# Optimization experiments

Measured on AMD Instinct MI355X. Metric: run time of the kernel, lower is better.

## Reference

```python
import jax, jax.numpy as jnp
import numpy as np

EMBED_DIM = 1024
NUM_HEADS = 16
BLOCK_SIZE = 128
GLOBAL_EVERY = 24


def make_block_sparse_mask(seq_len):
    # 0 where allowed, -inf where disallowed. Allowed iff same block, or
    # either position lies in a 'global' block (block index % global_every == 0).
    bi = jnp.arange(seq_len) // BLOCK_SIZE
    is_global = (bi % GLOBAL_EVERY) == 0
    allowed = (bi[:, None] == bi[None, :]) | is_global[:, None] | is_global[None, :]
    return jnp.where(allowed, 0.0, -jnp.inf).astype(jnp.float32)


def setup_inputs() -> dict:
    key = jax.random.key(0)
    k_x, k_w, k_wo = jax.random.split(key, 3)
    B, L, D = 1, 4096, EMBED_DIM
    x = jax.random.normal(k_x, (B, L, D), dtype=jnp.float32)
    # nn.MultiheadAttention params: packed in_proj [3D, D] + bias [3D], out_proj [D, D] + bias [D]
    w_qkv = jax.random.normal(k_w, (3 * D, D), dtype=jnp.float32) * 0.02
    b_qkv = jnp.zeros((3 * D,), dtype=jnp.float32)
    w_out = jax.random.normal(k_wo, (D, D), dtype=jnp.float32) * 0.02
    b_out = jnp.zeros((D,), dtype=jnp.float32)
    return {"x": x, "w_qkv": w_qkv, "b_qkv": b_qkv, "w_out": w_out, "b_out": b_out}


def reference(x, w_qkv, b_qkv, w_out, b_out):
    B, L, D = x.shape
    H = NUM_HEADS
    hd = D // H
    mask = make_block_sparse_mask(L)  # [L, L] additive
    qkv = x @ w_qkv.T + b_qkv  # [B, L, 3D]
    q, k, v = jnp.split(qkv, 3, axis=-1)
    # [B, H, L, hd]
    q = q.reshape(B, L, H, hd).transpose(0, 2, 1, 3)
    k = k.reshape(B, L, H, hd).transpose(0, 2, 1, 3)
    v = v.reshape(B, L, H, hd).transpose(0, 2, 1, 3)
    scale = 1.0 / jnp.sqrt(jnp.asarray(hd, dtype=x.dtype))
    scores = jnp.einsum('bhqd,bhkd->bhqk', q * scale, k) + mask  # [B, H, L, L]
    attn = jax.nn.softmax(scores, axis=-1)
    out = jnp.einsum('bhqk,bhkd->bhqd', attn, v)  # [B, H, L, hd]
    out = out.transpose(0, 2, 1, 3).reshape(B, L, D)
    return out @ w_out.T + b_out
```

## Files before the change

### kernel.cpp

```cpp
#include <hip/hip_runtime.h>
#include <hip/hip_bf16.h>
#include <math.h>


#define SEQ 4096
#define DIM 1024
#define NHEADS 16
#define HDIM 64
#define BS 128
#define ESTRIDE 136

using short8 = __attribute__((ext_vector_type(8))) short;
using floatx4 = __attribute__((ext_vector_type(4))) float;

__device__ __forceinline__ float bf2f(short s) {
  unsigned u = ((unsigned)(unsigned short)s) << 16;
  return __uint_as_float(u);
}

__device__ __forceinline__ unsigned pack_bf16(float a, float b) {
  __hip_bfloat16 ba = __float2bfloat16(a);
  __hip_bfloat16 bb = __float2bfloat16(b);
  return ((unsigned)*(unsigned short*)&bb << 16) | (unsigned)*(unsigned short*)&ba;
}

__device__ __forceinline__ void gld_lds16(const __hip_bfloat16* g, __hip_bfloat16* l) {
  __builtin_amdgcn_global_load_lds(
      (const __attribute__((address_space(1))) unsigned int*)g,
      (__attribute__((address_space(3))) unsigned int*)l, 16, 0, 0);
}

__global__ __launch_bounds__(256) void downcast3(
    const float* __restrict__ x, const float* __restrict__ wq,
    const float* __restrict__ wo, __hip_bfloat16* __restrict__ xd,
    __hip_bfloat16* __restrict__ wqd, __hip_bfloat16* __restrict__ wod) {
  int id = blockIdx.x;
  const float* src;
  __hip_bfloat16* dst;
  int base;
  if (id < 4096) { src = x; dst = xd; base = id; }
  else if (id < 7168) { src = wq; dst = wqd; base = id - 4096; }
  else { src = wo; dst = wod; base = id - 7168; }
  int i = (base * 256 + threadIdx.x) * 4;
  float4 v = *(const float4*)(src + i);
  __hip_bfloat16 b0 = __float2bfloat16(v.x);
  __hip_bfloat16 b1 = __float2bfloat16(v.y);
  __hip_bfloat16 b2 = __float2bfloat16(v.z);
  __hip_bfloat16 b3 = __float2bfloat16(v.w);
  ushort4 packed = {*(unsigned short*)&b0, *(unsigned short*)&b1,
                    *(unsigned short*)&b2, *(unsigned short*)&b3};
  *(ushort4*)(((unsigned short*)dst) + i) = packed;
}

__global__ __launch_bounds__(256) void gemm_qkv(const __hip_bfloat16* __restrict__ Amat,
                                                const __hip_bfloat16* __restrict__ Wmat,
                                                const float* __restrict__ Bias,
                                                __hip_bfloat16* __restrict__ qkv) {
  __shared__ __align__(16) char pool[128 * ESTRIDE * 2];
  __hip_bfloat16* Asmem = (__hip_bfloat16*)pool;
  __hip_bfloat16* Bsmem = (__hip_bfloat16*)(pool + 8192);
  __hip_bfloat16* Ep = (__hip_bfloat16*)pool;

  const int Kd = DIM;
  const int t = threadIdx.x;
  const int w = t >> 6;
  const int lane = t & 63;
  const int fr = lane & 15;
  const int quad = lane >> 4;
  const int wm = w >> 1, wn = w & 1;

  int id = blockIdx.x;
  int xcd = id & 7, j = id >> 3;
  int m_idx = xcd + (j & 3) * 8;
  int n_idx = j >> 2;
  const int m0 = m_idx * 128;
  const int n0 = n_idx * 128;
  const int s = n0 >> 10;
  const int cc0 = n0 & 1023;
  const bool vmode = (s == 2);

  const __hip_bfloat16* APtr = vmode ? Amat + (size_t)m0 * Kd : Wmat + (size_t)n0 * Kd;
  const __hip_bfloat16* BPtr = vmode ? Wmat + (size_t)n0 * Kd : Amat + (size_t)m0 * Kd;

  floatx4 acc[4][4];
#pragma unroll
  for (int i = 0; i < 4; ++i)
#pragma unroll
    for (int jj = 0; jj < 4; ++jj) acc[i][jj] = (floatx4){0.f, 0.f, 0.f, 0.f};

  for (int kk = 0; kk < Kd / 32; ++kk) {
#pragma unroll
    for (int jj = 0; jj < 2; ++jj) {
      int c = jj * 256 + t;
      int ldso = (jj * 256 + w * 64) * 8;
      gld_lds16(APtr + (size_t)(c >> 2) * Kd + kk * 32 + (c & 3) * 8, &Asmem[ldso]);
      gld_lds16(BPtr + (size_t)(c >> 2) * Kd + kk * 32 + (c & 3) * 8, &Bsmem[ldso]);
    }
    __syncthreads();
    short8 af[4], bf_[4];
#pragma unroll
    for (int mt = 0; mt < 4; ++mt)
      af[mt] = *(const short8*)&Asmem[(wm * 64 + mt * 16 + fr) * 32 + quad * 8];
#pragma unroll
    for (int nt = 0; nt < 4; ++nt)
      bf_[nt] = *(const short8*)&Bsmem[(wn * 64 + nt * 16 + fr) * 32 + quad * 8];
#pragma unroll
    for (int mt = 0; mt < 4; ++mt)
#pragma unroll
      for (int nt = 0; nt < 4; ++nt)
        acc[mt][nt] = __builtin_amdgcn_mfma_f32_16x16x32_bf16(af[mt], bf_[nt],
                                                              acc[mt][nt], 0, 0, 0);
    __syncthreads();
  }

#pragma unroll
  for (int nt = 0; nt < 4; ++nt) {
    int dcol = wn * 64 + nt * 16 + fr;
#pragma unroll
    for (int mt = 0; mt < 4; ++mt) {
      int drow0 = wm * 64 + mt * 16 + quad * 4;
      ushort4 pk;
      unsigned short* pks = (unsigned short*)&pk;
#pragma unroll
      for (int i = 0; i < 4; ++i) {
        __hip_bfloat16 bb = __float2bfloat16(acc[mt][nt][i]);
        pks[i] = *(unsigned short*)&bb;
      }
      *(ushort4*)&Ep[dcol * ESTRIDE + drow0] = pk;
    }
  }
  __syncthreads();

  if (!vmode) {
    __hip_bfloat16* dst = qkv + (size_t)s * SEQ * DIM;
#pragma unroll
    for (int rr = 0; rr < 8; ++rr) {
      int m = rr * 16 + (t >> 4);
      int ch = (t & 15) * 8;
      short8 v8 = *(const short8*)&Ep[m * ESTRIDE + ch];
      float4 b0 = *(const float4*)&Bias[n0 + ch];
      float4 b1 = *(const float4*)&Bias[n0 + ch + 4];
      float bb[8] = {b0.x, b0.y, b0.z, b0.w, b1.x, b1.y, b1.z, b1.w};
      short8 o8;
#pragma unroll
      for (int k = 0; k < 8; ++k) {
        __hip_bfloat16 ob = __float2bfloat16(bf2f(v8[k]) + bb[k]);
        o8[k] = *(short*)&ob;
      }
      *(short8*)&dst[(size_t)(m0 + m) * DIM + cc0 + ch] = o8;
    }
  } else {
    __hip_bfloat16* vt = qkv + 2ull * SEQ * DIM;
#pragma unroll
    for (int rr = 0; rr < 8; ++rr) {
      int nrow = rr * 16 + (t >> 4);
      int ch = (t & 15) * 8;
      float bv = Bias[n0 + nrow];
      short8 v8 = *(const short8*)&Ep[nrow * ESTRIDE + ch];
      short8 o8;
#pragma unroll
      for (int k = 0; k < 8; ++k) {
        __hip_bfloat16 ob = __float2bfloat16(bf2f(v8[k]) + bv);
        o8[k] = *(short*)&ob;
      }
      *(short8*)&vt[(size_t)(cc0 + nrow) * SEQ + m0 + ch] = o8;
    }
  }
}

__global__ __launch_bounds__(256) void gemm_out(const __hip_bfloat16* __restrict__ Amat,
                                                const __hip_bfloat16* __restrict__ Wmat,
                                                const float* __restrict__ Bias,
                                                float* __restrict__ out) {
  __shared__ __align__(16) __hip_bfloat16 Asmem[128 * 32];
  __shared__ __align__(16) __hip_bfloat16 Bsmem[64 * 32];
  const int Kd = DIM;
  const int t = threadIdx.x;
  const int w = t >> 6;
  const int lane = t & 63;
  const int fr = lane & 15;
  const int quad = lane >> 4;
  const int wm = w >> 1, wn = w & 1;
  int id = blockIdx.x;
  int xcd = id & 7, j = id >> 3;
  int m_idx = xcd + (j & 3) * 8;
  int n_idx = j >> 2;
  const int m0 = m_idx * 128;
  const int n0 = n_idx * 64;
  const __hip_bfloat16* Ablk = Amat + (size_t)m0 * Kd;
  const __hip_bfloat16* Bblk = Wmat + (size_t)n0 * Kd;
  floatx4 acc[4][2];
#pragma unroll
  for (int i = 0; i < 4; ++i)
#pragma unroll
    for (int jj = 0; jj < 2; ++jj) acc[i][jj] = (floatx4){0.f, 0.f, 0.f, 0.f};
  for (int kk = 0; kk < Kd / 32; ++kk) {
#pragma unroll
    for (int jj = 0; jj < 2; ++jj) {
      int c = jj * 256 + t;
      int ldso = (jj * 256 + w * 64) * 8;
      gld_lds16(Ablk + (size_t)(c >> 2) * Kd + kk * 32 + (c & 3) * 8, &Asmem[ldso]);
    }
    gld_lds16(Bblk + (size_t)(t >> 2) * Kd + kk * 32 + (t & 3) * 8, &Bsmem[t * 8]);
    __syncthreads();
    short8 af[4], bf_[2];
#pragma unroll
    for (int mt = 0; mt < 4; ++mt)
      af[mt] = *(const short8*)&Asmem[(wm * 64 + mt * 16 + fr) * 32 + quad * 8];
#pragma unroll
    for (int nt = 0; nt < 2; ++nt)
      bf_[nt] = *(const short8*)&Bsmem[(wn * 32 + nt * 16 + fr) * 32 + quad * 8];
#pragma unroll
    for (int mt = 0; mt < 4; ++mt)
#pragma unroll
      for (int nt = 0; nt < 2; ++nt)
        acc[mt][nt] = __builtin_amdgcn_mfma_f32_16x16x32_bf16(af[mt], bf_[nt],
                                                              acc[mt][nt], 0, 0, 0);
    __syncthreads();
  }
#pragma unroll
  for (int nt = 0; nt < 2; ++nt) {
    int n = n0 + wn * 32 + nt * 16 + fr;
    float bv = Bias[n];
#pragma unroll
    for (int mt = 0; mt < 4; ++mt) {
      int m = m0 + wm * 64 + mt * 16 + quad * 4;
#pragma unroll
      for (int i = 0; i < 4; ++i)
        out[(size_t)(m + i) * DIM + n] = acc[mt][nt][i] + bv;
    }
  }
}

__global__ __launch_bounds__(256) void attn_mfma(
    const __hip_bfloat16* __restrict__ qkv,
    __hip_bfloat16* __restrict__ aout,
    float* __restrict__ po, float* __restrict__ pm, float* __restrict__ pl) {
  __shared__ __align__(16) __hip_bfloat16 Kbuf[16 * 512];
  __shared__ __align__(16) __hip_bfloat16 Vbuf[16 * 512];
  const int h = blockIdx.y;
  const int wgid = blockIdx.x;
  const int t = threadIdx.x;
  const int wv = t >> 6;
  const int lane = t & 63;
  const int fr = lane & 15;
  const int quad = lane >> 4;

  int qb, q0, niter, slice = 0, pid = 0;
  bool direct;
  if (wgid < 60) {
    int nb = wgid >> 1;
    qb = (nb < 23) ? nb + 1 : nb + 2;
    q0 = qb * BS + (wgid & 1) * 64;
    niter = 3;
    direct = true;
  } else {
    int gi = wgid - 60;
    slice = gi & 7;
    int chunk = gi >> 3;
    qb = (chunk >> 1) * 24;
    q0 = qb * BS + (chunk & 1) * 64;
    niter = 4;
    direct = false;
    pid = (h * 4 + chunk) * 8 + slice;
  }

  const __hip_bfloat16* Q = qkv;
  const __hip_bfloat16* K = qkv + (size_t)SEQ * DIM;
  const __hip_bfloat16* Vt = qkv + 2ull * SEQ * DIM;

  short8 qa0, qa1;
  {
    const __hip_bfloat16* qp =
        Q + (size_t)(q0 + wv * 16 + fr) * DIM + h * HDIM + quad * 8;
    qa0 = *(const short8*)(qp);
    qa1 = *(const short8*)(qp + 32);
  }

  float mrow = -INFINITY, lsum = 0.f;
  floatx4 o[4];
#pragma unroll
  for (int i = 0; i < 4; ++i) o[i] = (floatx4){0.f, 0.f, 0.f, 0.f};

  for (int bi = 0; bi < niter; ++bi) {
    int kb = direct ? (bi == 0 ? 0 : (bi == 1 ? qb : 24)) : slice * 4 + bi;

    const __hip_bfloat16* Kg = K + (size_t)(kb * BS) * DIM + h * HDIM;
    const __hip_bfloat16* Vg = Vt + (size_t)(h * HDIM) * SEQ + kb * BS;
    __syncthreads();
#pragma unroll
    for (int rr = 0; rr < 4; ++rr) {
      int f = rr * 4 + wv;
      int nt = f >> 1, ks = f & 1;
      gld_lds16(Kg + (size_t)(nt * 16 + fr) * DIM + ks * 32 + quad * 8,
                &Kbuf[f * 512]);
      int nt2 = f >> 2, ks2 = f & 3;
      gld_lds16(Vg + (size_t)(nt2 * 16 + fr) * SEQ + ks2 * 32 + quad * 8,
                &Vbuf[f * 512]);
    }
    __syncthreads();

    floatx4 s[8];
#pragma unroll
    for (int nt = 0; nt < 8; ++nt) {
      short8 kf0 = *(const short8*)&Kbuf[(nt * 2 + 0) * 512 + lane * 8];
      short8 kf1 = *(const short8*)&Kbuf[(nt * 2 + 1) * 512 + lane * 8];
      floatx4 acc = {0.f, 0.f, 0.f, 0.f};
      acc = __builtin_amdgcn_mfma_f32_16x16x32_bf16(kf0, qa0, acc, 0, 0, 0);
      acc = __builtin_amdgcn_mfma_f32_16x16x32_bf16(kf1, qa1, acc, 0, 0, 0);
      s[nt] = acc;
    }
#pragma unroll
    for (int nt = 0; nt < 8; ++nt)
#pragma unroll
      for (int i = 0; i < 4; ++i) s[nt][i] *= 0.125f;

    float rmax = -INFINITY;
#pragma unroll
    for (int nt = 0; nt < 8; ++nt)
#pragma unroll
      for (int i = 0; i < 4; ++i) rmax = fmaxf(rmax, s[nt][i]);
    rmax = fmaxf(rmax, __shfl_xor(rmax, 16, 64));
    rmax = fmaxf(rmax, __shfl_xor(rmax, 32, 64));
    float newm = fmaxf(mrow, rmax);
    float alpha = __expf(mrow - newm);
    float psum = 0.f;
    unsigned pki[8][2];
#pragma unroll
    for (int nt = 0; nt < 8; ++nt) {
      float p0 = __expf(s[nt][0] - newm);
      float p1 = __expf(s[nt][1] - newm);
      float p2 = __expf(s[nt][2] - newm);
      float p3 = __expf(s[nt][3] - newm);
      psum += (p0 + p1) + (p2 + p3);
      pki[nt][0] = pack_bf16(p0, p1);
      pki[nt][1] = pack_bf16(p2, p3);
    }
    psum += __shfl_xor(psum, 16, 64);
    psum += __shfl_xor(psum, 32, 64);
    lsum = lsum * alpha + psum;
    mrow = newm;
#pragma unroll
    for (int nt2 = 0; nt2 < 4; ++nt2)
#pragma unroll
      for (int i = 0; i < 4; ++i) o[nt2][i] *= alpha;

    union { int w4[4]; short8 s8; } pw[4];
#pragma unroll
    for (int ks2 = 0; ks2 < 4; ++ks2) {
#pragma unroll
      for (int p = 0; p < 4; ++p) {
        int srcl = fr + ((((quad & 1) << 1) + (p >> 1)) << 4);
        int lo = __shfl((int)pki[2 * ks2][p & 1], srcl, 64);
        int hi = __shfl((int)pki[2 * ks2 + 1][p & 1], srcl, 64);
        pw[ks2].w4[p] = (quad & 2) ? hi : lo;
      }
    }

#pragma unroll
    for (int nt2 = 0; nt2 < 4; ++nt2) {
#pragma unroll
      for (int ks2 = 0; ks2 < 4; ++ks2) {
        short8 vb = *(const short8*)&Vbuf[(nt2 * 4 + ks2) * 512 + lane * 8];
        o[nt2] = __builtin_amdgcn_mfma_f32_16x16x32_bf16(vb, pw[ks2].s8, o[nt2], 0, 0, 0);
      }
    }
  }

  if (direct) {
    float inv = 1.f / lsum;
    __hip_bfloat16* orow = aout + (size_t)(q0 + wv * 16 + fr) * DIM + h * HDIM + quad * 4;
#pragma unroll
    for (int nt2 = 0; nt2 < 4; ++nt2) {
      ushort4 pk;
      unsigned short* pks = (unsigned short*)&pk;
#pragma unroll
      for (int i = 0; i < 4; ++i) {
        __hip_bfloat16 ob = __float2bfloat16(o[nt2][i] * inv);
        pks[i] = *(unsigned short*)&ob;
      }
      *(ushort4*)(orow + nt2 * 16) = pk;
    }
  } else {
    float* pob = po + (size_t)pid * 4096 + (wv * 16 + fr) * 64 + quad * 4;
#pragma unroll
    for (int nt2 = 0; nt2 < 4; ++nt2) {
      float4 v = {o[nt2][0], o[nt2][1], o[nt2][2], o[nt2][3]};
      *(float4*)(pob + nt2 * 16) = v;
    }
    if (quad == 0) {
      pm[pid * 64 + wv * 16 + fr] = mrow;
      pl[pid * 64 + wv * 16 + fr] = lsum;
    }
  }
}

__global__ __launch_bounds__(256) void combine(const float* __restrict__ po,
                                               const float* __restrict__ pm,
                                               const float* __restrict__ pl,
                                               __hip_bfloat16* __restrict__ aout) {
  int b = blockIdx.x;
  int h = b >> 2, chunk = b & 3;
  int t = threadIdx.x;
  int row = t >> 2;
  int d0 = (t & 3) * 16;

  float m8[8];
  float newm = -INFINITY;
#pragma unroll
  for (int s = 0; s < 8; ++s) {
    m8[s] = pm[(b * 8 + s) * 64 + row];
    newm = fmaxf(newm, m8[s]);
  }
  float wgt[8], lsum = 0.f;
#pragma unroll
  for (int s = 0; s < 8; ++s) {
    wgt[s] = __expf(m8[s] - newm);
    lsum += pl[(b * 8 + s) * 64 + row] * wgt[s];
  }
  float acc[16];
#pragma unroll
  for (int jj = 0; jj < 16; ++jj) acc[jj] = 0.f;
#pragma unroll
  for (int s = 0; s < 8; ++s) {
    const float* src = po + ((size_t)(b * 8 + s) * 4096) + row * 64 + d0;
#pragma unroll
    for (int j4 = 0; j4 < 4; ++j4) {
      float4 v = *(const float4*)(src + j4 * 4);
      acc[j4 * 4 + 0] += wgt[s] * v.x;
      acc[j4 * 4 + 1] += wgt[s] * v.y;
      acc[j4 * 4 + 2] += wgt[s] * v.z;
      acc[j4 * 4 + 3] += wgt[s] * v.w;
    }
  }
  float inv = 1.f / lsum;
  int qrow = (chunk >> 1) * 3072 + (chunk & 1) * 64 + row;
#pragma unroll
  for (int jj = 0; jj < 16; ++jj)
    aout[(size_t)qrow * DIM + h * HDIM + d0 + jj] = __float2bfloat16(acc[jj] * inv);
}

extern "C" void kernel_launch(void* const* d_in, const int* in_sizes, int n_in,
                              void* d_out, int out_size, void* d_ws, size_t ws_size,
                              hipStream_t stream) {
  const float* x = (const float*)d_in[0];
  const float* w_qkv = (const float*)d_in[1];
  const float* b_qkv = (const float*)d_in[2];
  const float* w_out = (const float*)d_in[3];
  const float* b_out = (const float*)d_in[4];
  float* out = (float*)d_out;

  char* wsb = (char*)d_ws;
  __hip_bfloat16* qkv_ws = (__hip_bfloat16*)(wsb);
  __hip_bfloat16* x_bf = (__hip_bfloat16*)(wsb + 24ull * 1024 * 1024);
  __hip_bfloat16* wqkv_bf = (__hip_bfloat16*)(wsb + 32ull * 1024 * 1024);
  __hip_bfloat16* wout_bf = (__hip_bfloat16*)(wsb + 38ull * 1024 * 1024);
  __hip_bfloat16* attn_ws = (__hip_bfloat16*)(wsb + 40ull * 1024 * 1024);
  float* po = (float*)(wsb + 24ull * 1024 * 1024);
  float* pm = (float*)(wsb + 32ull * 1024 * 1024);
  float* pl = (float*)(wsb + 32ull * 1024 * 1024 + 131072);

  dim3 blk(256);
  downcast3<<<dim3(8192), blk, 0, stream>>>(x, w_qkv, w_out, x_bf, wqkv_bf, wout_bf);
  gemm_qkv<<<dim3(768), blk, 0, stream>>>(x_bf, wqkv_bf, b_qkv, qkv_ws);
  attn_mfma<<<dim3(92, NHEADS), blk, 0, stream>>>(qkv_ws, attn_ws, po, pm, pl);
  combine<<<dim3(64), blk, 0, stream>>>(po, pm, pl, attn_ws);
  gemm_out<<<dim3(512), blk, 0, stream>>>(attn_ws, wout_bf, b_out, out);
}
```

Before: 174.5 us.

## Process 128 query rows per attention workgroup to reuse K/V tiles

Each attention workgroup now handles two 64-row query groups (a full 128-row block) against each loaded K/V tile instead of one, halving the grid from 92x16 to 46x16. This halves global-to-LDS traffic for K and V and the number of barriers per query row. Partial-result buffers and the combine kernel are re-indexed to the 128-row layout. In exchange, each workgroup needs more registers for the two accumulator sets and there are fewer workgroups, so occupancy and parallelism drop on a 256-CU device.

After: 178.5 us. 2.3% more time.

```diff
diff --git a/kernel.cpp b/kernel.cpp
--- a/kernel.cpp
+++ b/kernel.cpp
@@ -246,41 +246,45 @@
   const int fr = lane & 15;
   const int quad = lane >> 4;
 
-  int qb, q0, niter, slice = 0, pid = 0;
+  int qb, niter, slice = 0, pid = 0;
   bool direct;
-  if (wgid < 60) {
-    int nb = wgid >> 1;
-    qb = (nb < 23) ? nb + 1 : nb + 2;
-    q0 = qb * BS + (wgid & 1) * 64;
+  if (wgid < 30) {
+    qb = (wgid < 23) ? wgid + 1 : wgid + 2;
     niter = 3;
     direct = true;
   } else {
-    int gi = wgid - 60;
+    int gi = wgid - 30;
     slice = gi & 7;
-    int chunk = gi >> 3;
-    qb = (chunk >> 1) * 24;
-    q0 = qb * BS + (chunk & 1) * 64;
+    int qc = gi >> 3;
+    qb = qc * 24;
     niter = 4;
     direct = false;
-    pid = (h * 4 + chunk) * 8 + slice;
-  }
+    pid = (h * 2 + qc) * 8 + slice;
+  }
+  const int q0 = qb * BS;
 
   const __hip_bfloat16* Q = qkv;
   const __hip_bfloat16* K = qkv + (size_t)SEQ * DIM;
   const __hip_bfloat16* Vt = qkv + 2ull * SEQ * DIM;
 
-  short8 qa0, qa1;
+  short8 qaA0, qaA1, qaB0, qaB1;
   {
     const __hip_bfloat16* qp =
         Q + (size_t)(q0 + wv * 16 + fr) * DIM + h * HDIM + quad * 8;
-    qa0 = *(const short8*)(qp);
-    qa1 = *(const short8*)(qp + 32);
-  }
-
-  float mrow = -INFINITY, lsum = 0.f;
-  floatx4 o[4];
-#pragma unroll
-  for (int i = 0; i < 4; ++i) o[i] = (floatx4){0.f, 0.f, 0.f, 0.f};
+    qaA0 = *(const short8*)(qp);
+    qaA1 = *(const short8*)(qp + 32);
+    qp += (size_t)64 * DIM;
+    qaB0 = *(const short8*)(qp);
+    qaB1 = *(const short8*)(qp + 32);
+  }
+
+  float mA = -INFINITY, lA = 0.f, mB = -INFINITY, lB = 0.f;
+  floatx4 oA[4], oB[4];
+#pragma unroll
+  for (int i = 0; i < 4; ++i) {
+    oA[i] = (floatx4){0.f, 0.f, 0.f, 0.f};
+    oB[i] = (floatx4){0.f, 0.f, 0.f, 0.f};
+  }
 
   for (int bi = 0; bi < niter; ++bi) {
     int kb = direct ? (bi == 0 ? 0 : (bi == 1 ? qb : 24)) : slice * 4 + bi;
@@ -300,97 +304,117 @@
     }
     __syncthreads();
 
-    floatx4 s[8];
-#pragma unroll
-    for (int nt = 0; nt < 8; ++nt) {
-      short8 kf0 = *(const short8*)&Kbuf[(nt * 2 + 0) * 512 + lane * 8];
-      short8 kf1 = *(const short8*)&Kbuf[(nt * 2 + 1) * 512 + lane * 8];
-      floatx4 acc = {0.f, 0.f, 0.f, 0.f};
-      acc = __builtin_amdgcn_mfma_f32_16x16x32_bf16(kf0, qa0, acc, 0, 0, 0);
-      acc = __builtin_amdgcn_mfma_f32_16x16x32_bf16(kf1, qa1, acc, 0, 0, 0);
-      s[nt] = acc;
-    }
-#pragma unroll
-    for (int nt = 0; nt < 8; ++nt)
-#pragma unroll
-      for (int i = 0; i < 4; ++i) s[nt][i] *= 0.125f;
-
-    float rmax = -INFINITY;
-#pragma unroll
-    for (int nt = 0; nt < 8; ++nt)
-#pragma unroll
-      for (int i = 0; i < 4; ++i) rmax = fmaxf(rmax, s[nt][i]);
-    rmax = fmaxf(rmax, __shfl_xor(rmax, 16, 64));
-    rmax = fmaxf(rmax, __shfl_xor(rmax, 32, 64));
-    float newm = fmaxf(mrow, rmax);
-    float alpha = __expf(mrow - newm);
-    float psum = 0.f;
-    unsigned pki[8][2];
-#pragma unroll
-    for (int nt = 0; nt < 8; ++nt) {
-      float p0 = __expf(s[nt][0] - newm);
-      float p1 = __expf(s[nt][1] - newm);
-      float p2 = __expf(s[nt][2] - newm);
-      float p3 = __expf(s[nt][3] - newm);
-      psum += (p0 + p1) + (p2 + p3);
-      pki[nt][0] = pack_bf16(p0, p1);
-      pki[nt][1] = pack_bf16(p2, p3);
-    }
-    psum += __shfl_xor(psum, 16, 64);
-    psum += __shfl_xor(psum, 32, 64);
-    lsum = lsum * alpha + psum;
-    mrow = newm;
-#pragma unroll
-    for (int nt2 = 0; nt2 < 4; ++nt2)
-#pragma unroll
-      for (int i = 0; i < 4; ++i) o[nt2][i] *= alpha;
-
-    union { int w4[4]; short8 s8; } pw[4];
-#pragma unroll
-    for (int ks2 = 0; ks2 < 4; ++ks2) {
-#pragma unroll
-      for (int p = 0; p < 4; ++p) {
-        int srcl = fr + ((((quad & 1) << 1) + (p >> 1)) << 4);
-        int lo = __shfl((int)pki[2 * ks2][p & 1], srcl, 64);
-        int hi = __shfl((int)pki[2 * ks2 + 1][p & 1], srcl, 64);
-        pw[ks2].w4[p] = (quad & 2) ? hi : lo;
-      }
-    }
-
-#pragma unroll
-    for (int nt2 = 0; nt2 < 4; ++nt2) {
+#pragma unroll
+    for (int rg = 0; rg < 2; ++rg) {
+      short8 q0f = rg ? qaB0 : qaA0;
+      short8 q1f = rg ? qaB1 : qaA1;
+      float mrow = rg ? mB : mA;
+      float lsum = rg ? lB : lA;
+
+      floatx4 s[8];
+#pragma unroll
+      for (int nt = 0; nt < 8; ++nt) {
+        short8 kf0 = *(const short8*)&Kbuf[(nt * 2 + 0) * 512 + lane * 8];
+        short8 kf1 = *(const short8*)&Kbuf[(nt * 2 + 1) * 512 + lane * 8];
+        floatx4 acc = {0.f, 0.f, 0.f, 0.f};
+        acc = __builtin_amdgcn_mfma_f32_16x16x32_bf16(kf0, q0f, acc, 0, 0, 0);
+        acc = __builtin_amdgcn_mfma_f32_16x16x32_bf16(kf1, q1f, acc, 0, 0, 0);
+        s[nt] = acc;
+      }
+#pragma unroll
+      for (int nt = 0; nt < 8; ++nt)
+#pragma unroll
+        for (int i = 0; i < 4; ++i) s[nt][i] *= 0.125f;
+
+      float rmax = -INFINITY;
+#pragma unroll
+      for (int nt = 0; nt < 8; ++nt)
+#pragma unroll
+        for (int i = 0; i < 4; ++i) rmax = fmaxf(rmax, s[nt][i]);
+      rmax = fmaxf(rmax, __shfl_xor(rmax, 16, 64));
+      rmax = fmaxf(rmax, __shfl_xor(rmax, 32, 64));
+      float newm = fmaxf(mrow, rmax);
+      float alpha = __expf(mrow - newm);
+      float psum = 0.f;
+      unsigned pki[8][2];
+#pragma unroll
+      for (int nt = 0; nt < 8; ++nt) {
+        float p0 = __expf(s[nt][0] - newm);
+        float p1 = __expf(s[nt][1] - newm);
+        float p2 = __expf(s[nt][2] - newm);
+        float p3 = __expf(s[nt][3] - newm);
+        psum += (p0 + p1) + (p2 + p3);
+        pki[nt][0] = pack_bf16(p0, p1);
+        pki[nt][1] = pack_bf16(p2, p3);
+      }
+      psum += __shfl_xor(psum, 16, 64);
+      psum += __shfl_xor(psum, 32, 64);
+      lsum = lsum * alpha + psum;
+      mrow = newm;
+      if (rg) { mB = mrow; lB = lsum; } else { mA = mrow; lA = lsum; }
+
+#pragma unroll
+      for (int nt2 = 0; nt2 < 4; ++nt2)
+#pragma unroll
+        for (int i = 0; i < 4; ++i) {
+          if (rg) oB[nt2][i] *= alpha; else oA[nt2][i] *= alpha;
+        }
+
 #pragma unroll
       for (int ks2 = 0; ks2 < 4; ++ks2) {
-        short8 vb = *(const short8*)&Vbuf[(nt2 * 4 + ks2) * 512 + lane * 8];
-        o[nt2] = __builtin_amdgcn_mfma_f32_16x16x32_bf16(vb, pw[ks2].s8, o[nt2], 0, 0, 0);
+        union { int w4[4]; short8 s8; } pw;
+#pragma unroll
+        for (int p = 0; p < 4; ++p) {
+          int srcl = fr + ((((quad & 1) << 1) + (p >> 1)) << 4);
+          int lo = __shfl((int)pki[2 * ks2][p & 1], srcl, 64);
+          int hi = __shfl((int)pki[2 * ks2 + 1][p & 1], srcl, 64);
+          pw.w4[p] = (quad & 2) ? hi : lo;
+        }
+#pragma unroll
+        for (int nt2 = 0; nt2 < 4; ++nt2) {
+          short8 vb = *(const short8*)&Vbuf[(nt2 * 4 + ks2) * 512 + lane * 8];
+          if (rg)
+            oB[nt2] = __builtin_amdgcn_mfma_f32_16x16x32_bf16(vb, pw.s8, oB[nt2], 0, 0, 0);
+          else
+            oA[nt2] = __builtin_amdgcn_mfma_f32_16x16x32_bf16(vb, pw.s8, oA[nt2], 0, 0, 0);
+        }
       }
     }
   }
 
   if (direct) {
-    float inv = 1.f / lsum;
-    __hip_bfloat16* orow = aout + (size_t)(q0 + wv * 16 + fr) * DIM + h * HDIM + quad * 4;
-#pragma unroll
-    for (int nt2 = 0; nt2 < 4; ++nt2) {
-      ushort4 pk;
-      unsigned short* pks = (unsigned short*)&pk;
-#pragma unroll
-      for (int i = 0; i < 4; ++i) {
-        __hip_bfloat16 ob = __float2bfloat16(o[nt2][i] * inv);
-        pks[i] = *(unsigned short*)&ob;
-      }
-      *(ushort4*)(orow + nt2 * 16) = pk;
+#pragma unroll
+    for (int rg = 0; rg < 2; ++rg) {
+      float inv = 1.f / (rg ? lB : lA);
+      __hip_bfloat16* orow = aout +
+          (size_t)(q0 + rg * 64 + wv * 16 + fr) * DIM + h * HDIM + quad * 4;
+#pragma unroll
+      for (int nt2 = 0; nt2 < 4; ++nt2) {
+        ushort4 pk;
+        unsigned short* pks = (unsigned short*)&pk;
+#pragma unroll
+        for (int i = 0; i < 4; ++i) {
+          float ov = rg ? oB[nt2][i] : oA[nt2][i];
+          __hip_bfloat16 ob = __float2bfloat16(ov * inv);
+          pks[i] = *(unsigned short*)&ob;
+        }
+        *(ushort4*)(orow + nt2 * 16) = pk;
+      }
     }
   } else {
-    float* pob = po + (size_t)pid * 4096 + (wv * 16 + fr) * 64 + quad * 4;
-#pragma unroll
-    for (int nt2 = 0; nt2 < 4; ++nt2) {
-      float4 v = {o[nt2][0], o[nt2][1], o[nt2][2], o[nt2][3]};
-      *(float4*)(pob + nt2 * 16) = v;
-    }
-    if (quad == 0) {
-      pm[pid * 64 + wv * 16 + fr] = mrow;
-      pl[pid * 64 + wv * 16 + fr] = lsum;
+#pragma unroll
+    for (int rg = 0; rg < 2; ++rg) {
+      float* pob = po + (size_t)pid * 8192 + (rg * 64 + wv * 16 + fr) * 64 + quad * 4;
+#pragma unroll
+      for (int nt2 = 0; nt2 < 4; ++nt2) {
+        floatx4 ov = rg ? oB[nt2] : oA[nt2];
+        float4 v = {ov[0], ov[1], ov[2], ov[3]};
+        *(float4*)(pob + nt2 * 16) = v;
+      }
+      if (quad == 0) {
+        pm[pid * 128 + rg * 64 + wv * 16 + fr] = rg ? mB : mA;
+        pl[pid * 128 + rg * 64 + wv * 16 + fr] = rg ? lB : lA;
+      }
     }
   }
 }
@@ -399,31 +423,32 @@
                                                const float* __restrict__ pm,
                                                const float* __restrict__ pl,
                                                __hip_bfloat16* __restrict__ aout) {
-  int b = blockIdx.x;
-  int h = b >> 2, chunk = b & 3;
+  int b2 = blockIdx.x;
+  int h = b2 >> 2, qc = (b2 >> 1) & 1, half = b2 & 1;
+  int bb = h * 2 + qc;
   int t = threadIdx.x;
-  int row = t >> 2;
+  int row = half * 64 + (t >> 2);
   int d0 = (t & 3) * 16;
 
   float m8[8];
   float newm = -INFINITY;
 #pragma unroll
   for (int s = 0; s < 8; ++s) {
-    m8[s] = pm[(b * 8 + s) * 64 + row];
+    m8[s] = pm[(bb * 8 + s) * 128 + row];
     newm = fmaxf(newm, m8[s]);
   }
   float wgt[8], lsum = 0.f;
 #pragma unroll
   for (int s = 0; s < 8; ++s) {
     wgt[s] = __expf(m8[s] - newm);
-    lsum += pl[(b * 8 + s) * 64 + row] * wgt[s];
+    lsum += pl[(bb * 8 + s) * 128 + row] * wgt[s];
   }
   float acc[16];
 #pragma unroll
   for (int jj = 0; jj < 16; ++jj) acc[jj] = 0.f;
 #pragma unroll
   for (int s = 0; s < 8; ++s) {
-    const float* src = po + ((size_t)(b * 8 + s) * 4096) + row * 64 + d0;
+    const float* src = po + ((size_t)(bb * 8 + s) * 8192) + row * 64 + d0;
 #pragma unroll
     for (int j4 = 0; j4 < 4; ++j4) {
       float4 v = *(const float4*)(src + j4 * 4);
@@ -434,7 +459,7 @@
     }
   }
   float inv = 1.f / lsum;
-  int qrow = (chunk >> 1) * 3072 + (chunk & 1) * 64 + row;
+  int qrow = qc * 3072 + row;
 #pragma unroll
   for (int jj = 0; jj < 16; ++jj)
     aout[(size_t)qrow * DIM + h * HDIM + d0 + jj] = __float2bfloat16(acc[jj] * inv);
@@ -463,7 +488,7 @@
   dim3 blk(256);
   downcast3<<<dim3(8192), blk, 0, stream>>>(x, w_qkv, w_out, x_bf, wqkv_bf, wout_bf);
   gemm_qkv<<<dim3(768), blk, 0, stream>>>(x_bf, wqkv_bf, b_qkv, qkv_ws);
-  attn_mfma<<<dim3(92, NHEADS), blk, 0, stream>>>(qkv_ws, attn_ws, po, pm, pl);
+  attn_mfma<<<dim3(46, NHEADS), blk, 0, stream>>>(qkv_ws, attn_ws, po, pm, pl);
   combine<<<dim3(64), blk, 0, stream>>>(po, pm, pl, attn_ws);
   gemm_out<<<dim3(512), blk, 0, stream>>>(attn_ws, wout_bf, b_out, out);
 }
```
